# Kernel tuning notes

Hardware: AMD Instinct MI355X
Metric: run time of the kernel (lower is better)

The kernel has to match this reference:

```python
import jax, jax.numpy as jnp
import numpy as np

H = 64  # hidden size
I = 1   # input size


def setup_inputs() -> dict:
    key = jax.random.key(0)
    ks = jax.random.split(key, 7)
    B, T = 4096, 512
    s_ih = 1.0 / np.sqrt(H)
    x = jax.random.normal(ks[0], (B, T, I), dtype=jnp.float32)
    # torch nn.GRU params: weight_ih [3H, I], weight_hh [3H, H], biases [3H]
    W_ih = jax.random.uniform(ks[1], (3 * H, I), minval=-s_ih, maxval=s_ih, dtype=jnp.float32)
    W_hh = jax.random.uniform(ks[2], (3 * H, H), minval=-s_ih, maxval=s_ih, dtype=jnp.float32)
    b_ih = jax.random.uniform(ks[3], (3 * H,), minval=-s_ih, maxval=s_ih, dtype=jnp.float32)
    b_hh = jax.random.uniform(ks[4], (3 * H,), minval=-s_ih, maxval=s_ih, dtype=jnp.float32)
    # final Linear(64, 1)
    W_out = jax.random.uniform(ks[5], (1, H), minval=-s_ih, maxval=s_ih, dtype=jnp.float32)
    b_out = jax.random.uniform(ks[6], (1,), minval=-s_ih, maxval=s_ih, dtype=jnp.float32)
    return {"x": x, "W_ih": W_ih, "W_hh": W_hh, "b_ih": b_ih, "b_hh": b_hh,
            "W_out": W_out, "b_out": b_out}


def _gru_last_hidden(x, W_ih, W_hh, b_ih, b_hh):
    B, T, _ = x.shape
    # precompute input projections for all timesteps: [B, T, 3H]
    xp = jnp.einsum('bti,gi->btg', x, W_ih) + b_ih
    xp = jnp.swapaxes(xp, 0, 1)  # [T, B, 3H]
    Whr, Whz, Whn = W_hh[:H], W_hh[H:2 * H], W_hh[2 * H:]
    bhr, bhz, bhn = b_hh[:H], b_hh[H:2 * H], b_hh[2 * H:]

    def step(h, xt):
        xr, xz, xn = xt[:, :H], xt[:, H:2 * H], xt[:, 2 * H:]
        r = jax.nn.sigmoid(xr + h @ Whr.T + bhr)
        z = jax.nn.sigmoid(xz + h @ Whz.T + bhz)
        n = jnp.tanh(xn + r * (h @ Whn.T + bhn))
        h_new = (1.0 - z) * n + z * h
        return h_new, None

    h0 = jnp.zeros((B, H), dtype=x.dtype)
    h_last, _ = jax.lax.scan(step, h0, xp)
    return h_last


def reference(x, W_ih, W_hh, b_ih, b_hh, W_out, b_out):
    h_last = _gru_last_hidden(x, W_ih, W_hh, b_ih, b_hh)
    return h_last @ W_out.T + b_out  # [B, 1]
```

## Files before the change

kernel.cpp:

```cpp
#include <hip/hip_runtime.h>
#include <stdint.h>

#define TT 512
#define BT 8
#define XSTR 516

typedef float    f32x4 __attribute__((ext_vector_type(4)));
typedef float    f32x2 __attribute__((ext_vector_type(2)));
typedef short    s16x8 __attribute__((ext_vector_type(8)));
typedef __fp16   h16x2 __attribute__((ext_vector_type(2)));
typedef _Float16 f16x8 __attribute__((ext_vector_type(8)));

#define MFMA_F16(A, B, C) \
    __builtin_amdgcn_mfma_f32_16x16x32_f16( \
        __builtin_bit_cast(f16x8, (A)), (B), (C), 0, 0, 0)

#define LOG2E  1.442695040888963f
#define LOG2E2 2.885390081777927f

__global__ __launch_bounds__(256, 2) void gru_scan_kernel(
    const float* __restrict__ x,
    const float* __restrict__ Wih,
    const float* __restrict__ Whh,
    const float* __restrict__ bih,
    const float* __restrict__ bhh,
    const float* __restrict__ Wout,
    const float* __restrict__ bout,
    float* __restrict__ out)
{
    __shared__ __align__(16) float xs[BT * XSTR];
    __shared__ __align__(16) short hbuf[2][1024];
    __shared__ float outp[4][BT];

    const int tid  = threadIdx.x;
    const int w    = tid >> 6;
    const int L    = tid & 63;
    const int n16  = L & 15;
    const int quad = L >> 4;
    const int q    = w * 16 + n16;
    const int b0   = blockIdx.x * BT;

    #pragma unroll
    for (int k = 0; k < 4; ++k) {
        int idx = tid + k * 256;
        int row = idx >> 7;
        int t4  = idx & 127;
        f32x4 v = *(const f32x4*)(x + (size_t)(b0 + row) * TT + t4 * 4);
        *(f32x4*)(xs + row * XSTR + t4 * 4) = v;
    }
    {
        f32x4* hb = (f32x4*)hbuf;
        f32x4 zv = {0.f, 0.f, 0.f, 0.f};
        hb[tid] = zv;
    }

    const float wr2   = -LOG2E  * Wih[q];
    const float wz2   = -LOG2E  * Wih[64 + q];
    const float wn2   =  LOG2E2 * Wih[128 + q];
    const float bR2   = -LOG2E  * (bih[q]      + bhh[q]);
    const float bZ2   = -LOG2E  * (bih[64 + q] + bhh[64 + q]);
    const float bN2   =  LOG2E2 * bhh[128 + q];
    const float bihn2 =  LOG2E2 * bih[128 + q];
    const float wo    = Wout[q];

    const f32x4 bR4 = {bR2, bR2, bR2, bR2};
    const f32x4 bZ4 = {bZ2, bZ2, bZ2, bZ2};
    const f32x4 bN4 = {bN2, bN2, bN2, bN2};

    f16x8 Bf[3][2];
    #pragma unroll
    for (int g = 0; g < 3; ++g) {
        const float sg = (g == 2) ? LOG2E2 : -LOG2E;
        #pragma unroll
        for (int c = 0; c < 2; ++c) {
            const float* p = Whh + ((g * 64 + q) * 64 + c * 32 + quad * 8);
            #pragma unroll
            for (int j = 0; j < 8; ++j)
                Bf[g][c][j] = (_Float16)(p[j] * sg);
        }
    }

    float hD[2] = {0.f, 0.f};

    const int kg   = q >> 3;
    const int sxor = (kg & 1) * 4;
    int waddr[2];
    #pragma unroll
    for (int p = 0; p < 2; ++p)
        waddr[p] = (kg * 16 + ((p * 4 + quad) ^ sxor)) * 8 + (q & 7);

    const int permx = ((n16 & 3) * 4 + (n16 >> 2)) ^ ((quad & 1) * 4);
    const int rslot = quad * 16 + permx;

    const s16x8* hbv = (const s16x8*)hbuf;
    const float* xrow0 = xs + (quad * 2) * XSTR;
    const float* xrow1 = xrow0 + XSTR;

    if ((blockIdx.x >> 8) & 1) __builtin_amdgcn_s_sleep(6);

    auto step = [&](int cur, f32x2 xv) {
        __syncthreads();

        s16x8 A0 = hbv[cur * 128 +  0 + rslot];
        s16x8 A1 = hbv[cur * 128 + 64 + rslot];

        f32x4 aR = MFMA_F16(A0, Bf[0][0], bR4);
        aR       = MFMA_F16(A1, Bf[0][1], aR);
        f32x4 aN = MFMA_F16(A0, Bf[2][0], bN4);
        aN       = MFMA_F16(A1, Bf[2][1], aN);
        f32x4 aZ = MFMA_F16(A0, Bf[1][0], bZ4);
        aZ       = MFMA_F16(A1, Bf[1][1], aZ);

        short* wh = (short*)hbuf + (cur ^ 1) * 1024;

        f32x2 aRp = {aR[0], aR[1]};
        f32x2 aZp = {aZ[0], aZ[1]};
        f32x2 aNp = {aN[0], aN[1]};
        f32x2 hp  = {hD[0], hD[1]};

        f32x2 ar = xv * wr2 + aRp;
        f32x2 Er = {__builtin_amdgcn_exp2f(ar[0]), __builtin_amdgcn_exp2f(ar[1])};
        f32x2 DR = Er + 1.0f;
        f32x2 r  = {__builtin_amdgcn_rcpf(DR[0]), __builtin_amdgcn_rcpf(DR[1])};
        f32x2 az = xv * wz2 + aZp;
        f32x2 Ez = {__builtin_amdgcn_exp2f(az[0]), __builtin_amdgcn_exp2f(az[1])};
        f32x2 DZ = Ez + 1.0f;
        f32x2 xn = xv * wn2 + bihn2;
        f32x2 an = r * aNp + xn;
        f32x2 En = {__builtin_amdgcn_exp2f(an[0]), __builtin_amdgcn_exp2f(an[1])};
        f32x2 DN = En + 1.0f;
        f32x2 P  = DZ * DN;
        f32x2 iq = {__builtin_amdgcn_rcpf(P[0]), __builtin_amdgcn_rcpf(P[1])};
        f32x2 z  = iq * DN;
        f32x2 rn = iq * DZ;
        f32x2 n  = rn * -2.0f + 1.0f;
        f32x2 hn = z * (hp - n) + n;

        hD[0] = hn[0]; hD[1] = hn[1];

        h16x2 hpk = __builtin_amdgcn_cvt_pkrtz(hn[0], hn[1]);
        unsigned upk = __builtin_bit_cast(unsigned, hpk);
        wh[waddr[0]] = (short)(upk & 0xffffu);
        wh[waddr[1]] = (short)(upk >> 16);
    };

    for (int t = 0; t < TT; t += 4) {
        f32x4 xa = *(const f32x4*)(xrow0 + t);
        f32x4 xb = *(const f32x4*)(xrow1 + t);
        step(0, f32x2{xa[0], xb[0]});
        step(1, f32x2{xa[1], xb[1]});
        step(0, f32x2{xa[2], xb[2]});
        step(1, f32x2{xa[3], xb[3]});
    }

    float p0 = hD[0] * wo;
    float p1 = hD[1] * wo;
    #pragma unroll
    for (int mask = 1; mask <= 8; mask <<= 1) {
        p0 += __shfl_xor(p0, mask, 64);
        p1 += __shfl_xor(p1, mask, 64);
    }
    if (n16 == 0) {
        outp[w][quad * 2]     = p0;
        outp[w][quad * 2 + 1] = p1;
    }
    __syncthreads();
    if (tid < BT) {
        out[b0 + tid] = outp[0][tid] + outp[1][tid] + outp[2][tid] + outp[3][tid] + bout[0];
    }
}

extern "C" void kernel_launch(void* const* d_in, const int* in_sizes, int n_in,
                              void* d_out, int out_size, void* d_ws, size_t ws_size,
                              hipStream_t stream) {
    (void)in_sizes; (void)n_in; (void)d_ws; (void)ws_size; (void)out_size;
    const float* x    = (const float*)d_in[0];
    const float* Wih  = (const float*)d_in[1];
    const float* Whh  = (const float*)d_in[2];
    const float* bih  = (const float*)d_in[3];
    const float* bhh  = (const float*)d_in[4];
    const float* Wout = (const float*)d_in[5];
    const float* bout = (const float*)d_in[6];
    float* out = (float*)d_out;

    gru_scan_kernel<<<dim3(4096 / BT), dim3(256), 0, stream>>>(
        x, Wih, Whh, bih, bhh, Wout, bout, out);
}
```

Baseline: 196.4 us.

## Halve batch rows per block to four and double blocks per CU

Each block now handles 4 batch rows instead of 8, so every lane computes one hidden element instead of two. The grid doubles to 1024 blocks, launch bounds allow 4 blocks per CU, and the sleep staggering across block groups widens to four phases. The R and N gate MFMA chains are split into two independent accumulators to shorten the dependency chain, and the input projection is hoisted out of the step. This trades per-step work and latency for more concurrent blocks to hide the serial recurrence latency; MFMA rows are now only partly used, and the extra blocks add barrier overhead.

```diff
diff --git a/kernel.cpp b/kernel.cpp
--- a/kernel.cpp
+++ b/kernel.cpp
@@ -2,13 +2,11 @@
 #include <stdint.h>
 
 #define TT 512
-#define BT 8
+#define BT 4
 #define XSTR 516
 
 typedef float    f32x4 __attribute__((ext_vector_type(4)));
-typedef float    f32x2 __attribute__((ext_vector_type(2)));
 typedef short    s16x8 __attribute__((ext_vector_type(8)));
-typedef __fp16   h16x2 __attribute__((ext_vector_type(2)));
 typedef _Float16 f16x8 __attribute__((ext_vector_type(8)));
 
 #define MFMA_F16(A, B, C) \
@@ -18,7 +16,7 @@
 #define LOG2E  1.442695040888963f
 #define LOG2E2 2.885390081777927f
 
-__global__ __launch_bounds__(256, 2) void gru_scan_kernel(
+__global__ __launch_bounds__(256, 4) void gru_scan_kernel(
     const float* __restrict__ x,
     const float* __restrict__ Wih,
     const float* __restrict__ Whh,
@@ -29,7 +27,7 @@
     float* __restrict__ out)
 {
     __shared__ __align__(16) float xs[BT * XSTR];
-    __shared__ __align__(16) short hbuf[2][1024];
+    __shared__ __align__(16) short hbuf[2][256];
     __shared__ float outp[4][BT];
 
     const int tid  = threadIdx.x;
@@ -41,18 +39,14 @@
     const int b0   = blockIdx.x * BT;
 
     #pragma unroll
-    for (int k = 0; k < 4; ++k) {
+    for (int k = 0; k < 2; ++k) {
         int idx = tid + k * 256;
         int row = idx >> 7;
         int t4  = idx & 127;
         f32x4 v = *(const f32x4*)(x + (size_t)(b0 + row) * TT + t4 * 4);
         *(f32x4*)(xs + row * XSTR + t4 * 4) = v;
     }
-    {
-        f32x4* hb = (f32x4*)hbuf;
-        f32x4 zv = {0.f, 0.f, 0.f, 0.f};
-        hb[tid] = zv;
-    }
+    ((unsigned*)hbuf)[tid] = 0u;
 
     const float wr2   = -LOG2E  * Wih[q];
     const float wz2   = -LOG2E  * Wih[64 + q];
@@ -63,9 +57,10 @@
     const float bihn2 =  LOG2E2 * bih[128 + q];
     const float wo    = Wout[q];
 
-    const f32x4 bR4 = {bR2, bR2, bR2, bR2};
-    const f32x4 bZ4 = {bZ2, bZ2, bZ2, bZ2};
-    const f32x4 bN4 = {bN2, bN2, bN2, bN2};
+    const f32x4 bR4   = {bR2, bR2, bR2, bR2};
+    const f32x4 bZ4   = {bZ2, bZ2, bZ2, bZ2};
+    const f32x4 bN4   = {bN2, bN2, bN2, bN2};
+    const f32x4 zero4 = {0.f, 0.f, 0.f, 0.f};
 
     f16x8 Bf[3][2];
     #pragma unroll
@@ -80,90 +75,79 @@
         }
     }
 
-    float hD[2] = {0.f, 0.f};
+    float hD  = 0.f;
+    float hm1 = -1.f;
 
-    const int kg   = q >> 3;
-    const int sxor = (kg & 1) * 4;
-    int waddr[2];
-    #pragma unroll
-    for (int p = 0; p < 2; ++p)
-        waddr[p] = (kg * 16 + ((p * 4 + quad) ^ sxor)) * 8 + (q & 7);
+    const int waddr = ((q >> 3) * 4 + quad) * 8 + (q & 7);
+    const int rslot = quad * 4 + (n16 >> 2);
+    const s16x8* hbv = (const s16x8*)hbuf;
+    const float* xrow = xs + quad * XSTR;
 
-    const int permx = ((n16 & 3) * 4 + (n16 >> 2)) ^ ((quad & 1) * 4);
-    const int rslot = quad * 16 + permx;
+    {
+        const int ph = (blockIdx.x >> 8) & 3;
+        if      (ph == 1) __builtin_amdgcn_s_sleep(2);
+        else if (ph == 2) __builtin_amdgcn_s_sleep(4);
+        else if (ph == 3) __builtin_amdgcn_s_sleep(6);
+    }
 
-    const s16x8* hbv = (const s16x8*)hbuf;
-    const float* xrow0 = xs + (quad * 2) * XSTR;
-    const float* xrow1 = xrow0 + XSTR;
-
-    if ((blockIdx.x >> 8) & 1) __builtin_amdgcn_s_sleep(6);
-
-    auto step = [&](int cur, f32x2 xv) {
+    auto step = [&](int cur, float xr_, float xz_, float xn_) {
         __syncthreads();
 
-        s16x8 A0 = hbv[cur * 128 +  0 + rslot];
-        s16x8 A1 = hbv[cur * 128 + 64 + rslot];
+        s16x8 A0 = hbv[cur * 32 +      rslot];
+        s16x8 A1 = hbv[cur * 32 + 16 + rslot];
 
-        f32x4 aR = MFMA_F16(A0, Bf[0][0], bR4);
-        aR       = MFMA_F16(A1, Bf[0][1], aR);
-        f32x4 aN = MFMA_F16(A0, Bf[2][0], bN4);
-        aN       = MFMA_F16(A1, Bf[2][1], aN);
-        f32x4 aZ = MFMA_F16(A0, Bf[1][0], bZ4);
-        aZ       = MFMA_F16(A1, Bf[1][1], aZ);
+        f32x4 aRa = MFMA_F16(A0, Bf[0][0], bR4);
+        f32x4 aRb = MFMA_F16(A1, Bf[0][1], zero4);
+        f32x4 aNa = MFMA_F16(A0, Bf[2][0], bN4);
+        f32x4 aNb = MFMA_F16(A1, Bf[2][1], zero4);
+        f32x4 aZ  = MFMA_F16(A0, Bf[1][0], bZ4);
+        aZ        = MFMA_F16(A1, Bf[1][1], aZ);
 
-        short* wh = (short*)hbuf + (cur ^ 1) * 1024;
+        float ar  = (xr_ + aRa[0]) + aRb[0];
+        float Er  = __builtin_amdgcn_exp2f(ar);
+        float DR  = Er + 1.0f;
+        float r   = __builtin_amdgcn_rcpf(DR);
+        float aN0 = aNa[0] + aNb[0];
+        float az  = xz_ + aZ[0];
+        float Ez  = __builtin_amdgcn_exp2f(az);
+        float DZ  = Ez + 1.0f;
+        float an  = r * aN0 + xn_;
+        float En  = __builtin_amdgcn_exp2f(an);
+        float DN  = En + 1.0f;
+        float P   = DZ * DN;
+        float iq  = __builtin_amdgcn_rcpf(P);
+        float rn  = iq * DZ;
+        float z   = iq * DN;
+        float n   = rn * -2.0f + 1.0f;
+        float s   = rn *  2.0f + hm1;
+        float hn  = z * s + n;
 
-        f32x2 aRp = {aR[0], aR[1]};
-        f32x2 aZp = {aZ[0], aZ[1]};
-        f32x2 aNp = {aN[0], aN[1]};
-        f32x2 hp  = {hD[0], hD[1]};
+        hD  = hn;
+        hm1 = hn - 1.0f;
 
-        f32x2 ar = xv * wr2 + aRp;
-        f32x2 Er = {__builtin_amdgcn_exp2f(ar[0]), __builtin_amdgcn_exp2f(ar[1])};
-        f32x2 DR = Er + 1.0f;
-        f32x2 r  = {__builtin_amdgcn_rcpf(DR[0]), __builtin_amdgcn_rcpf(DR[1])};
-        f32x2 az = xv * wz2 + aZp;
-        f32x2 Ez = {__builtin_amdgcn_exp2f(az[0]), __builtin_amdgcn_exp2f(az[1])};
-        f32x2 DZ = Ez + 1.0f;
-        f32x2 xn = xv * wn2 + bihn2;
-        f32x2 an = r * aNp + xn;
-        f32x2 En = {__builtin_amdgcn_exp2f(an[0]), __builtin_amdgcn_exp2f(an[1])};
-        f32x2 DN = En + 1.0f;
-        f32x2 P  = DZ * DN;
-        f32x2 iq = {__builtin_amdgcn_rcpf(P[0]), __builtin_amdgcn_rcpf(P[1])};
-        f32x2 z  = iq * DN;
-        f32x2 rn = iq * DZ;
-        f32x2 n  = rn * -2.0f + 1.0f;
-        f32x2 hn = z * (hp - n) + n;
-
-        hD[0] = hn[0]; hD[1] = hn[1];
-
-        h16x2 hpk = __builtin_amdgcn_cvt_pkrtz(hn[0], hn[1]);
-        unsigned upk = __builtin_bit_cast(unsigned, hpk);
-        wh[waddr[0]] = (short)(upk & 0xffffu);
-        wh[waddr[1]] = (short)(upk >> 16);
+        short* wh = (short*)hbuf + (cur ^ 1) * 256;
+        _Float16 hf = (_Float16)hn;
+        wh[waddr] = __builtin_bit_cast(short, hf);
     };
 
     for (int t = 0; t < TT; t += 4) {
-        f32x4 xa = *(const f32x4*)(xrow0 + t);
-        f32x4 xb = *(const f32x4*)(xrow1 + t);
-        step(0, f32x2{xa[0], xb[0]});
-        step(1, f32x2{xa[1], xb[1]});
-        step(0, f32x2{xa[2], xb[2]});
-        step(1, f32x2{xa[3], xb[3]});
+        f32x4 xa = *(const f32x4*)(xrow + t);
+        float xr0 = xa[0] * wr2, xz0 = xa[0] * wz2, xn0 = xa[0] * wn2 + bihn2;
+        float xr1 = xa[1] * wr2, xz1 = xa[1] * wz2, xn1 = xa[1] * wn2 + bihn2;
+        float xr2 = xa[2] * wr2, xz2 = xa[2] * wz2, xn2 = xa[2] * wn2 + bihn2;
+        float xr3 = xa[3] * wr2, xz3 = xa[3] * wz2, xn3 = xa[3] * wn2 + bihn2;
+        step(0, xr0, xz0, xn0);
+        step(1, xr1, xz1, xn1);
+        step(0, xr2, xz2, xn2);
+        step(1, xr3, xz3, xn3);
     }
 
-    float p0 = hD[0] * wo;
-    float p1 = hD[1] * wo;
-    #pragma unroll
-    for (int mask = 1; mask <= 8; mask <<= 1) {
-        p0 += __shfl_xor(p0, mask, 64);
-        p1 += __shfl_xor(p1, mask, 64);
-    }
-    if (n16 == 0) {
-        outp[w][quad * 2]     = p0;
-        outp[w][quad * 2 + 1] = p1;
-    }
+    float p = hD * wo;
+    p += __shfl_xor(p, 1, 64);
+    p += __shfl_xor(p, 2, 64);
+    p += __shfl_xor(p, 4, 64);
+    p += __shfl_xor(p, 8, 64);
+    if (n16 == 0) outp[w][quad] = p;
     __syncthreads();
     if (tid < BT) {
         out[b0 + tid] = outp[0][tid] + outp[1][tid] + outp[2][tid] + outp[3][tid] + bout[0];
```

Result: slower. 254.0 us (+29.3%).

## Ping-pong two batch streams per block to overlap MFMA with gate math

Applied to the files above, without the earlier changes.

Each block now handles 16 batch rows with 512 threads, split into two 4-wave groups that each own 8 rows and their own hidden-state buffer. The groups alternate phases: while one runs the MFMA matrix products, the other runs the elementwise gate math, with a barrier between phases. The goal is to hide MFMA latency behind the transcendental-heavy vector work. It also splits the MFMA accumulations into two independent chains and reworks the h update algebra. The cost is two block-wide barriers per step, with half the grid's block count at twice the block size.

```diff
diff --git a/kernel.cpp b/kernel.cpp
--- a/kernel.cpp
+++ b/kernel.cpp
@@ -2,7 +2,7 @@
 #include <stdint.h>
 
 #define TT 512
-#define BT 8
+#define BTW 16
 #define XSTR 516
 
 typedef float    f32x4 __attribute__((ext_vector_type(4)));
@@ -18,7 +18,7 @@
 #define LOG2E  1.442695040888963f
 #define LOG2E2 2.885390081777927f
 
-__global__ __launch_bounds__(256, 2) void gru_scan_kernel(
+__global__ __launch_bounds__(512, 2) void gru_scan_kernel(
     const float* __restrict__ x,
     const float* __restrict__ Wih,
     const float* __restrict__ Whh,
@@ -28,31 +28,31 @@
     const float* __restrict__ bout,
     float* __restrict__ out)
 {
-    __shared__ __align__(16) float xs[BT * XSTR];
-    __shared__ __align__(16) short hbuf[2][1024];
-    __shared__ float outp[4][BT];
+    __shared__ __align__(16) float xs[BTW * XSTR];
+    __shared__ __align__(16) short hbufs[2][1024];
+    __shared__ float outp[8][8];
 
     const int tid  = threadIdx.x;
     const int w    = tid >> 6;
     const int L    = tid & 63;
     const int n16  = L & 15;
     const int quad = L >> 4;
-    const int q    = w * 16 + n16;
-    const int b0   = blockIdx.x * BT;
+    const int isP  = (w < 4);
+    const int sw   = isP ? 0 : 1;
+    const int q    = (w & 3) * 16 + n16;
+    const int b0   = blockIdx.x * BTW;
+    const int bs   = sw * 8;
 
     #pragma unroll
     for (int k = 0; k < 4; ++k) {
-        int idx = tid + k * 256;
+        int idx = tid + k * 512;
         int row = idx >> 7;
         int t4  = idx & 127;
         f32x4 v = *(const f32x4*)(x + (size_t)(b0 + row) * TT + t4 * 4);
         *(f32x4*)(xs + row * XSTR + t4 * 4) = v;
     }
-    {
-        f32x4* hb = (f32x4*)hbuf;
-        f32x4 zv = {0.f, 0.f, 0.f, 0.f};
-        hb[tid] = zv;
-    }
+    ((unsigned*)hbufs)[tid]       = 0u;
+    ((unsigned*)hbufs)[tid + 512] = 0u;
 
     const float wr2   = -LOG2E  * Wih[q];
     const float wz2   = -LOG2E  * Wih[64 + q];
@@ -63,9 +63,10 @@
     const float bihn2 =  LOG2E2 * bih[128 + q];
     const float wo    = Wout[q];
 
-    const f32x4 bR4 = {bR2, bR2, bR2, bR2};
-    const f32x4 bZ4 = {bZ2, bZ2, bZ2, bZ2};
-    const f32x4 bN4 = {bN2, bN2, bN2, bN2};
+    const f32x4 bR4   = {bR2, bR2, bR2, bR2};
+    const f32x4 bZ4   = {bZ2, bZ2, bZ2, bZ2};
+    const f32x4 bN4   = {bN2, bN2, bN2, bN2};
+    const f32x4 zero4 = {0.f, 0.f, 0.f, 0.f};
 
     f16x8 Bf[3][2];
     #pragma unroll
@@ -80,7 +81,8 @@
         }
     }
 
-    float hD[2] = {0.f, 0.f};
+    float hD0 = 0.f, hD1 = 0.f;
+    f32x2 hm1 = {-1.f, -1.f};
 
     const int kg   = q >> 3;
     const int sxor = (kg & 1) * 4;
@@ -92,69 +94,80 @@
     const int permx = ((n16 & 3) * 4 + (n16 >> 2)) ^ ((quad & 1) * 4);
     const int rslot = quad * 16 + permx;
 
-    const s16x8* hbv = (const s16x8*)hbuf;
-    const float* xrow0 = xs + (quad * 2) * XSTR;
+    short* myh = hbufs[sw];
+    const s16x8* hbv = (const s16x8*)myh;
+    const float* xrow0 = xs + (bs + quad * 2) * XSTR;
     const float* xrow1 = xrow0 + XSTR;
 
-    if ((blockIdx.x >> 8) & 1) __builtin_amdgcn_s_sleep(6);
-
-    auto step = [&](int cur, f32x2 xv) {
-        __syncthreads();
-
-        s16x8 A0 = hbv[cur * 128 +  0 + rslot];
-        s16x8 A1 = hbv[cur * 128 + 64 + rslot];
-
-        f32x4 aR = MFMA_F16(A0, Bf[0][0], bR4);
-        aR       = MFMA_F16(A1, Bf[0][1], aR);
-        f32x4 aN = MFMA_F16(A0, Bf[2][0], bN4);
-        aN       = MFMA_F16(A1, Bf[2][1], aN);
-        f32x4 aZ = MFMA_F16(A0, Bf[1][0], bZ4);
-        aZ       = MFMA_F16(A1, Bf[1][1], aZ);
-
-        short* wh = (short*)hbuf + (cur ^ 1) * 1024;
-
-        f32x2 aRp = {aR[0], aR[1]};
-        f32x2 aZp = {aZ[0], aZ[1]};
-        f32x2 aNp = {aN[0], aN[1]};
-        f32x2 hp  = {hD[0], hD[1]};
-
-        f32x2 ar = xv * wr2 + aRp;
+    f32x4 accRa, accRb, accNa, accNb, accZa, accZb;
+
+    auto rm = [&]() {
+        s16x8 A0 = hbv[rslot];
+        s16x8 A1 = hbv[64 + rslot];
+        accRa = MFMA_F16(A0, Bf[0][0], bR4);
+        accRb = MFMA_F16(A1, Bf[0][1], zero4);
+        accNa = MFMA_F16(A0, Bf[2][0], bN4);
+        accNb = MFMA_F16(A1, Bf[2][1], zero4);
+        accZa = MFMA_F16(A0, Bf[1][0], bZ4);
+        accZb = MFMA_F16(A1, Bf[1][1], zero4);
+    };
+
+    auto vw = [&](f32x2 xv) {
+        f32x2 aR = {accRa[0] + accRb[0], accRa[1] + accRb[1]};
+        f32x2 aN = {accNa[0] + accNb[0], accNa[1] + accNb[1]};
+        f32x2 aZ = {accZa[0] + accZb[0], accZa[1] + accZb[1]};
+
+        f32x2 ar = xv * wr2 + aR;
         f32x2 Er = {__builtin_amdgcn_exp2f(ar[0]), __builtin_amdgcn_exp2f(ar[1])};
         f32x2 DR = Er + 1.0f;
         f32x2 r  = {__builtin_amdgcn_rcpf(DR[0]), __builtin_amdgcn_rcpf(DR[1])};
-        f32x2 az = xv * wz2 + aZp;
+        f32x2 xn = xv * wn2 + bihn2;
+        f32x2 an = r * aN + xn;
+        f32x2 En = {__builtin_amdgcn_exp2f(an[0]), __builtin_amdgcn_exp2f(an[1])};
+        f32x2 DN = En + 1.0f;
+        f32x2 az = xv * wz2 + aZ;
         f32x2 Ez = {__builtin_amdgcn_exp2f(az[0]), __builtin_amdgcn_exp2f(az[1])};
         f32x2 DZ = Ez + 1.0f;
-        f32x2 xn = xv * wn2 + bihn2;
-        f32x2 an = r * aNp + xn;
-        f32x2 En = {__builtin_amdgcn_exp2f(an[0]), __builtin_amdgcn_exp2f(an[1])};
-        f32x2 DN = En + 1.0f;
         f32x2 P  = DZ * DN;
         f32x2 iq = {__builtin_amdgcn_rcpf(P[0]), __builtin_amdgcn_rcpf(P[1])};
         f32x2 z  = iq * DN;
         f32x2 rn = iq * DZ;
         f32x2 n  = rn * -2.0f + 1.0f;
-        f32x2 hn = z * (hp - n) + n;
-
-        hD[0] = hn[0]; hD[1] = hn[1];
+        f32x2 s  = rn *  2.0f + hm1;
+        f32x2 hn = z * s + n;
+
+        hD0 = hn[0]; hD1 = hn[1];
+        hm1 = hn - 1.0f;
 
         h16x2 hpk = __builtin_amdgcn_cvt_pkrtz(hn[0], hn[1]);
         unsigned upk = __builtin_bit_cast(unsigned, hpk);
-        wh[waddr[0]] = (short)(upk & 0xffffu);
-        wh[waddr[1]] = (short)(upk >> 16);
+        myh[waddr[0]] = (short)(upk & 0xffffu);
+        myh[waddr[1]] = (short)(upk >> 16);
     };
 
+    __syncthreads();
+
+    if (isP) rm();
+
+    f32x4 xa = *(const f32x4*)(xrow0);
+    f32x4 xb = *(const f32x4*)(xrow1);
     for (int t = 0; t < TT; t += 4) {
-        f32x4 xa = *(const f32x4*)(xrow0 + t);
-        f32x4 xb = *(const f32x4*)(xrow1 + t);
-        step(0, f32x2{xa[0], xb[0]});
-        step(1, f32x2{xa[1], xb[1]});
-        step(0, f32x2{xa[2], xb[2]});
-        step(1, f32x2{xa[3], xb[3]});
-    }
-
-    float p0 = hD[0] * wo;
-    float p1 = hD[1] * wo;
+        const int tn = (t + 4 < TT) ? t + 4 : 0;
+        f32x4 xan = *(const f32x4*)(xrow0 + tn);
+        f32x4 xbn = *(const f32x4*)(xrow1 + tn);
+        #pragma unroll
+        for (int j = 0; j < 4; ++j) {
+            f32x2 xv = {xa[j], xb[j]};
+            __syncthreads();
+            if (isP) vw(xv); else rm();
+            __syncthreads();
+            if (isP) rm(); else vw(xv);
+        }
+        xa = xan; xb = xbn;
+    }
+
+    float p0 = hD0 * wo;
+    float p1 = hD1 * wo;
     #pragma unroll
     for (int mask = 1; mask <= 8; mask <<= 1) {
         p0 += __shfl_xor(p0, mask, 64);
@@ -165,8 +178,11 @@
         outp[w][quad * 2 + 1] = p1;
     }
     __syncthreads();
-    if (tid < BT) {
-        out[b0 + tid] = outp[0][tid] + outp[1][tid] + outp[2][tid] + outp[3][tid] + bout[0];
+    if (tid < BTW) {
+        int ss = tid >> 3;
+        int c  = tid & 7;
+        out[b0 + tid] = outp[ss * 4 + 0][c] + outp[ss * 4 + 1][c] +
+                        outp[ss * 4 + 2][c] + outp[ss * 4 + 3][c] + bout[0];
     }
 }
 
@@ -183,6 +199,6 @@
     const float* bout = (const float*)d_in[6];
     float* out = (float*)d_out;
 
-    gru_scan_kernel<<<dim3(4096 / BT), dim3(256), 0, stream>>>(
+    gru_scan_kernel<<<dim3(4096 / BTW), dim3(512), 0, stream>>>(
         x, Wih, Whh, bih, bhh, Wout, bout, out);
 }
```

New measurement: 282.7 us. +43.9%, slower.

## Process 16 batch rows per block using full MFMA M dimension

Applied to the files above, without the earlier changes.

Doubles the batch rows per workgroup from 8 to 16, so every row of the 16x16 MFMA output is a real batch element and each lane updates four hidden states per step. The grid halves to 256 blocks. The K-split MFMA accumulations are now independent chains summed afterwards, the LDS swizzle for h is reworked, the h update is restated with a carried h-1 term, and the staggered s_sleep is removed. The aim is to halve the number of blocks and barriered timesteps per batch element. The cost is more VALU and transcendental work per step, fewer blocks for latency hiding, and a launch bound lowered to 1.

```diff
diff --git a/kernel.cpp b/kernel.cpp
--- a/kernel.cpp
+++ b/kernel.cpp
@@ -2,11 +2,10 @@
 #include <stdint.h>
 
 #define TT 512
-#define BT 8
+#define BTW 16
 #define XSTR 516
 
 typedef float    f32x4 __attribute__((ext_vector_type(4)));
-typedef float    f32x2 __attribute__((ext_vector_type(2)));
 typedef short    s16x8 __attribute__((ext_vector_type(8)));
 typedef __fp16   h16x2 __attribute__((ext_vector_type(2)));
 typedef _Float16 f16x8 __attribute__((ext_vector_type(8)));
@@ -18,7 +17,7 @@
 #define LOG2E  1.442695040888963f
 #define LOG2E2 2.885390081777927f
 
-__global__ __launch_bounds__(256, 2) void gru_scan_kernel(
+__global__ __launch_bounds__(256, 1) void gru_scan_kernel(
     const float* __restrict__ x,
     const float* __restrict__ Wih,
     const float* __restrict__ Whh,
@@ -28,9 +27,9 @@
     const float* __restrict__ bout,
     float* __restrict__ out)
 {
-    __shared__ __align__(16) float xs[BT * XSTR];
+    __shared__ __align__(16) float xs[BTW * XSTR];
     __shared__ __align__(16) short hbuf[2][1024];
-    __shared__ float outp[4][BT];
+    __shared__ float outp[4][BTW];
 
     const int tid  = threadIdx.x;
     const int w    = tid >> 6;
@@ -38,10 +37,10 @@
     const int n16  = L & 15;
     const int quad = L >> 4;
     const int q    = w * 16 + n16;
-    const int b0   = blockIdx.x * BT;
-
-    #pragma unroll
-    for (int k = 0; k < 4; ++k) {
+    const int b0   = blockIdx.x * BTW;
+
+    #pragma unroll
+    for (int k = 0; k < 8; ++k) {
         int idx = tid + k * 256;
         int row = idx >> 7;
         int t4  = idx & 127;
@@ -49,9 +48,8 @@
         *(f32x4*)(xs + row * XSTR + t4 * 4) = v;
     }
     {
-        f32x4* hb = (f32x4*)hbuf;
-        f32x4 zv = {0.f, 0.f, 0.f, 0.f};
-        hb[tid] = zv;
+        unsigned* hz = (unsigned*)hbuf;
+        hz[tid] = 0u; hz[tid + 256] = 0u; hz[tid + 512] = 0u; hz[tid + 768] = 0u;
     }
 
     const float wr2   = -LOG2E  * Wih[q];
@@ -63,9 +61,10 @@
     const float bihn2 =  LOG2E2 * bih[128 + q];
     const float wo    = Wout[q];
 
-    const f32x4 bR4 = {bR2, bR2, bR2, bR2};
-    const f32x4 bZ4 = {bZ2, bZ2, bZ2, bZ2};
-    const f32x4 bN4 = {bN2, bN2, bN2, bN2};
+    const f32x4 bR4   = {bR2, bR2, bR2, bR2};
+    const f32x4 bZ4   = {bZ2, bZ2, bZ2, bZ2};
+    const f32x4 bN4   = {bN2, bN2, bN2, bN2};
+    const f32x4 zero4 = {0.f, 0.f, 0.f, 0.f};
 
     f16x8 Bf[3][2];
     #pragma unroll
@@ -80,92 +79,109 @@
         }
     }
 
-    float hD[2] = {0.f, 0.f};
-
-    const int kg   = q >> 3;
-    const int sxor = (kg & 1) * 4;
-    int waddr[2];
-    #pragma unroll
-    for (int p = 0; p < 2; ++p)
-        waddr[p] = (kg * 16 + ((p * 4 + quad) ^ sxor)) * 8 + (q & 7);
-
-    const int permx = ((n16 & 3) * 4 + (n16 >> 2)) ^ ((quad & 1) * 4);
-    const int rslot = quad * 16 + permx;
+    const int slot0 = n16 * 8 + ( quad      ^ (n16 & 7));
+    const int slot1 = n16 * 8 + ((quad + 4) ^ (n16 & 7));
+    int wa[4];
+    #pragma unroll
+    for (int r = 0; r < 4; ++r) {
+        int bq = quad * 4 + r;
+        wa[r] = bq * 64 + (((q >> 3) ^ (bq & 7)) * 8) + (q & 7);
+    }
 
     const s16x8* hbv = (const s16x8*)hbuf;
-    const float* xrow0 = xs + (quad * 2) * XSTR;
-    const float* xrow1 = xrow0 + XSTR;
-
-    if ((blockIdx.x >> 8) & 1) __builtin_amdgcn_s_sleep(6);
-
-    auto step = [&](int cur, f32x2 xv) {
+    const float* xr0 = xs + (quad * 4 + 0) * XSTR;
+    const float* xr1 = xs + (quad * 4 + 1) * XSTR;
+    const float* xr2 = xs + (quad * 4 + 2) * XSTR;
+    const float* xr3 = xs + (quad * 4 + 3) * XSTR;
+
+    f32x4 hlast = {0.f, 0.f, 0.f, 0.f};
+    f32x4 hm1   = {-1.f, -1.f, -1.f, -1.f};
+
+    auto step = [&](int cur, f32x4 xv) {
         __syncthreads();
 
-        s16x8 A0 = hbv[cur * 128 +  0 + rslot];
-        s16x8 A1 = hbv[cur * 128 + 64 + rslot];
-
-        f32x4 aR = MFMA_F16(A0, Bf[0][0], bR4);
-        aR       = MFMA_F16(A1, Bf[0][1], aR);
-        f32x4 aN = MFMA_F16(A0, Bf[2][0], bN4);
-        aN       = MFMA_F16(A1, Bf[2][1], aN);
-        f32x4 aZ = MFMA_F16(A0, Bf[1][0], bZ4);
-        aZ       = MFMA_F16(A1, Bf[1][1], aZ);
-
+        s16x8 A0 = hbv[cur * 128 + slot0];
+        s16x8 A1 = hbv[cur * 128 + slot1];
+
+        f32x4 accRa = MFMA_F16(A0, Bf[0][0], bR4);
+        f32x4 accRb = MFMA_F16(A1, Bf[0][1], zero4);
+        f32x4 accNa = MFMA_F16(A0, Bf[2][0], bN4);
+        f32x4 accNb = MFMA_F16(A1, Bf[2][1], zero4);
+        f32x4 accZa = MFMA_F16(A0, Bf[1][0], bZ4);
+        f32x4 accZb = MFMA_F16(A1, Bf[1][1], zero4);
+
+        f32x4 aR = accRa + accRb;
+        f32x4 aN = accNa + accNb;
+        f32x4 aZ = accZa + accZb;
+
+        f32x4 ar = xv * wr2 + aR;
+        f32x4 Er = {__builtin_amdgcn_exp2f(ar[0]), __builtin_amdgcn_exp2f(ar[1]),
+                    __builtin_amdgcn_exp2f(ar[2]), __builtin_amdgcn_exp2f(ar[3])};
+        f32x4 DR = Er + 1.0f;
+        f32x4 r  = {__builtin_amdgcn_rcpf(DR[0]), __builtin_amdgcn_rcpf(DR[1]),
+                    __builtin_amdgcn_rcpf(DR[2]), __builtin_amdgcn_rcpf(DR[3])};
+        f32x4 xn = xv * wn2 + bihn2;
+        f32x4 an = r * aN + xn;
+        f32x4 En = {__builtin_amdgcn_exp2f(an[0]), __builtin_amdgcn_exp2f(an[1]),
+                    __builtin_amdgcn_exp2f(an[2]), __builtin_amdgcn_exp2f(an[3])};
+        f32x4 DN = En + 1.0f;
+        f32x4 az = xv * wz2 + aZ;
+        f32x4 Ez = {__builtin_amdgcn_exp2f(az[0]), __builtin_amdgcn_exp2f(az[1]),
+                    __builtin_amdgcn_exp2f(az[2]), __builtin_amdgcn_exp2f(az[3])};
+        f32x4 DZ = Ez + 1.0f;
+        f32x4 P  = DZ * DN;
+        f32x4 iq = {__builtin_amdgcn_rcpf(P[0]), __builtin_amdgcn_rcpf(P[1]),
+                    __builtin_amdgcn_rcpf(P[2]), __builtin_amdgcn_rcpf(P[3])};
+        f32x4 z  = iq * DN;
+        f32x4 rn = iq * DZ;
+        f32x4 n  = rn * -2.0f + 1.0f;
+        f32x4 s  = rn *  2.0f + hm1;
+        f32x4 hn = z * s + n;
+
+        hlast = hn;
+        hm1   = hn - 1.0f;
+
+        h16x2 pk01 = __builtin_amdgcn_cvt_pkrtz(hn[0], hn[1]);
+        h16x2 pk23 = __builtin_amdgcn_cvt_pkrtz(hn[2], hn[3]);
+        unsigned u01 = __builtin_bit_cast(unsigned, pk01);
+        unsigned u23 = __builtin_bit_cast(unsigned, pk23);
         short* wh = (short*)hbuf + (cur ^ 1) * 1024;
-
-        f32x2 aRp = {aR[0], aR[1]};
-        f32x2 aZp = {aZ[0], aZ[1]};
-        f32x2 aNp = {aN[0], aN[1]};
-        f32x2 hp  = {hD[0], hD[1]};
-
-        f32x2 ar = xv * wr2 + aRp;
-        f32x2 Er = {__builtin_amdgcn_exp2f(ar[0]), __builtin_amdgcn_exp2f(ar[1])};
-        f32x2 DR = Er + 1.0f;
-        f32x2 r  = {__builtin_amdgcn_rcpf(DR[0]), __builtin_amdgcn_rcpf(DR[1])};
-        f32x2 az = xv * wz2 + aZp;
-        f32x2 Ez = {__builtin_amdgcn_exp2f(az[0]), __builtin_amdgcn_exp2f(az[1])};
-        f32x2 DZ = Ez + 1.0f;
-        f32x2 xn = xv * wn2 + bihn2;
-        f32x2 an = r * aNp + xn;
-        f32x2 En = {__builtin_amdgcn_exp2f(an[0]), __builtin_amdgcn_exp2f(an[1])};
-        f32x2 DN = En + 1.0f;
-        f32x2 P  = DZ * DN;
-        f32x2 iq = {__builtin_amdgcn_rcpf(P[0]), __builtin_amdgcn_rcpf(P[1])};
-        f32x2 z  = iq * DN;
-        f32x2 rn = iq * DZ;
-        f32x2 n  = rn * -2.0f + 1.0f;
-        f32x2 hn = z * (hp - n) + n;
-
-        hD[0] = hn[0]; hD[1] = hn[1];
-
-        h16x2 hpk = __builtin_amdgcn_cvt_pkrtz(hn[0], hn[1]);
-        unsigned upk = __builtin_bit_cast(unsigned, hpk);
-        wh[waddr[0]] = (short)(upk & 0xffffu);
-        wh[waddr[1]] = (short)(upk >> 16);
+        wh[wa[0]] = (short)(u01 & 0xffffu);
+        wh[wa[1]] = (short)(u01 >> 16);
+        wh[wa[2]] = (short)(u23 & 0xffffu);
+        wh[wa[3]] = (short)(u23 >> 16);
     };
 
     for (int t = 0; t < TT; t += 4) {
-        f32x4 xa = *(const f32x4*)(xrow0 + t);
-        f32x4 xb = *(const f32x4*)(xrow1 + t);
-        step(0, f32x2{xa[0], xb[0]});
-        step(1, f32x2{xa[1], xb[1]});
-        step(0, f32x2{xa[2], xb[2]});
-        step(1, f32x2{xa[3], xb[3]});
-    }
-
-    float p0 = hD[0] * wo;
-    float p1 = hD[1] * wo;
+        f32x4 xa0 = *(const f32x4*)(xr0 + t);
+        f32x4 xa1 = *(const f32x4*)(xr1 + t);
+        f32x4 xa2 = *(const f32x4*)(xr2 + t);
+        f32x4 xa3 = *(const f32x4*)(xr3 + t);
+        step(0, f32x4{xa0[0], xa1[0], xa2[0], xa3[0]});
+        step(1, f32x4{xa0[1], xa1[1], xa2[1], xa3[1]});
+        step(0, f32x4{xa0[2], xa1[2], xa2[2], xa3[2]});
+        step(1, f32x4{xa0[3], xa1[3], xa2[3], xa3[3]});
+    }
+
+    float p0 = hlast[0] * wo;
+    float p1 = hlast[1] * wo;
+    float p2 = hlast[2] * wo;
+    float p3 = hlast[3] * wo;
     #pragma unroll
     for (int mask = 1; mask <= 8; mask <<= 1) {
         p0 += __shfl_xor(p0, mask, 64);
         p1 += __shfl_xor(p1, mask, 64);
+        p2 += __shfl_xor(p2, mask, 64);
+        p3 += __shfl_xor(p3, mask, 64);
     }
     if (n16 == 0) {
-        outp[w][quad * 2]     = p0;
-        outp[w][quad * 2 + 1] = p1;
+        outp[w][quad * 4 + 0] = p0;
+        outp[w][quad * 4 + 1] = p1;
+        outp[w][quad * 4 + 2] = p2;
+        outp[w][quad * 4 + 3] = p3;
     }
     __syncthreads();
-    if (tid < BT) {
+    if (tid < BTW) {
         out[b0 + tid] = outp[0][tid] + outp[1][tid] + outp[2][tid] + outp[3][tid] + bout[0];
     }
 }
@@ -183,6 +199,6 @@
     const float* bout = (const float*)d_in[6];
     float* out = (float*)d_out;
 
-    gru_scan_kernel<<<dim3(4096 / BT), dim3(256), 0, stream>>>(
+    gru_scan_kernel<<<dim3(4096 / BTW), dim3(256), 0, stream>>>(
         x, Wih, Whh, bih, bhh, Wout, bout, out);
 }
```

After: 255.7 us. +30.2%, slower.
